# Kernel optimization log

Hardware: AMD Instinct MI355X
Metric: run time of the kernel (lower is better)

Reference implementation:

```python
import jax, jax.numpy as jnp
import numpy as np

T, B, F = 256, 128, 1600
H1, H2, H3 = 60, 15, 10   # MLP dims
GH = 5                    # GRU hidden size


def setup_inputs() -> dict:
    key = jax.random.key(0)
    ks = jax.random.split(key, 24)
    s = 0.1
    inp = {
        "X":   jax.random.normal(ks[0], (T, B, F), jnp.float32),
        "W1":  jax.random.normal(ks[1], (H1, F), jnp.float32) * s,
        "b1":  jax.random.normal(ks[2], (H1,), jnp.float32) * s,
        "W2":  jax.random.normal(ks[3], (H2, H1), jnp.float32) * s,
        "b2":  jax.random.normal(ks[4], (H2,), jnp.float32) * s,
        "W3":  jax.random.normal(ks[5], (H3, H2), jnp.float32) * s,
        "b3":  jax.random.normal(ks[6], (H3,), jnp.float32) * s,
    }
    in_sizes = [H3, GH, GH]
    k = 7
    for l in range(3):
        inp[f"w_ih{l}"] = jax.random.normal(ks[k], (3 * GH, in_sizes[l]), jnp.float32) * s; k += 1
        inp[f"w_hh{l}"] = jax.random.normal(ks[k], (3 * GH, GH), jnp.float32) * s; k += 1
        inp[f"b_ih{l}"] = jax.random.normal(ks[k], (3 * GH,), jnp.float32) * s; k += 1
        inp[f"b_hh{l}"] = jax.random.normal(ks[k], (3 * GH,), jnp.float32) * s; k += 1
    inp["Wout"] = jax.random.normal(ks[k], (1, GH), jnp.float32) * s; k += 1
    inp["bout"] = jax.random.normal(ks[k], (1,), jnp.float32) * s
    return inp


def _gru_layer(x, w_ih, w_hh, b_ih, b_hh):
    # x: (Bb, Tt, I). Precompute input-side gates for all timesteps.
    gi = jnp.einsum('bti,gi->btg', x, w_ih) + b_ih  # (Bb, Tt, 3H)

    def step(h_prev, gi_t):
        gh = h_prev @ w_hh.T + b_hh                 # (Bb, 3H)
        ir, iz, in_ = jnp.split(gi_t, 3, axis=-1)
        hr, hz, hn = jnp.split(gh, 3, axis=-1)
        r = jax.nn.sigmoid(ir + hr)
        z = jax.nn.sigmoid(iz + hz)
        n = jnp.tanh(in_ + r * hn)
        h = (1.0 - z) * n + z * h_prev
        return h, h

    h0 = jnp.zeros((x.shape[0], w_hh.shape[1]), x.dtype)
    _, ys = jax.lax.scan(step, h0, jnp.swapaxes(gi, 0, 1))  # (Tt, Bb, H)
    return jnp.swapaxes(ys, 0, 1)                            # (Bb, Tt, H)


def reference(X, W1, b1, W2, b2, W3, b3,
              w_ih0, w_hh0, b_ih0, b_hh0,
              w_ih1, w_hh1, b_ih1, b_hh1,
              w_ih2, w_hh2, b_ih2, b_hh2,
              Wout, bout):
    x = jnp.transpose(X, (1, 0, 2))        # (B, T, 1600): GRU batch_first layout
    h = jnp.tanh(x @ W1.T + b1)
    h = jnp.tanh(h @ W2.T + b2)
    h = h @ W3.T + b3                      # (B, T, 10) -- no activation after last MLP layer
    seq = h
    for p in ((w_ih0, w_hh0, b_ih0, b_hh0),
              (w_ih1, w_hh1, b_ih1, b_hh1),
              (w_ih2, w_hh2, b_ih2, b_hh2)):
        seq = _gru_layer(seq, *p)          # (B, T, 5)
    y = jnp.swapaxes(seq, 0, 1)            # (T, B, 5)
    y = y @ Wout.T + bout                  # (T, B, 1)
    return jnp.swapaxes(y, -1, -2)         # (T, 1, B)
```

## Files before the change

### kernel.cpp

```cpp
#include <hip/hip_runtime.h>
#include <hip/hip_bf16.h>


#define T_DIM 256
#define B_DIM 128
#define F_DIM 1600
#define H1_DIM 60
#define H2_DIM 15
#define H3_DIM 10
#define GH 5
#define NSTEP 50
#define CT 32
#define NCH (T_DIM / CT)

#define DPP_SHR5  0x115
#define DPP_SHR10 0x11A

typedef __attribute__((ext_vector_type(8))) short bf16x8;
typedef __attribute__((ext_vector_type(4))) float f32x4;

__device__ __forceinline__ float fast_tanh(float x) {
    float e = __expf(2.0f * x);
    return 1.0f - __fdividef(2.0f, e + 1.0f);
}
__device__ __forceinline__ float fast_sigmoid(float x) {
    return __fdividef(1.0f, 1.0f + __expf(-x));
}
__device__ __forceinline__ ushort f2bf_rn(float x) {
    uint u = __float_as_uint(x);
    u += 0x7fffu + ((u >> 16) & 1u);
    return (ushort)(u >> 16);
}
template <int CTRL>
__device__ __forceinline__ float dppf(float v) {
    return __int_as_float(
        __builtin_amdgcn_mov_dpp(__float_as_int(v), CTRL, 0xf, 0xf, true));
}
__device__ __forceinline__ float bperm(int addr, float v) {
    return __int_as_float(__builtin_amdgcn_ds_bpermute(addr, __float_as_int(v)));
}

__global__ __launch_bounds__(256) void pack_w1_kernel(
    const float* __restrict__ W1, ushort* __restrict__ Wp)
{
    const int s  = blockIdx.x;
    const int t  = threadIdx.x;
    const int nf = t >> 6;
    const int l  = t & 63;
    const int n  = nf * 16 + (l & 15);
    const int g  = l >> 4;

    ushort hi[8], lo[8];
#pragma unroll
    for (int j = 0; j < 8; ++j) {
        const int k = s * 32 + g * 8 + j;
        const float v = (n < H1_DIM) ? W1[n * F_DIM + k] : 0.0f;
        const ushort h = f2bf_rn(v);
        const float hf = __uint_as_float(((uint)h) << 16);
        const float r  = v - hf;
        hi[j] = h;
        lo[j] = (ushort)(__float_as_uint(r) >> 16);
    }
    ushort* dst = Wp + ((size_t)(s * 8 + nf * 2)) * 512 + l * 8;
#pragma unroll
    for (int j = 0; j < 8; ++j) dst[j] = hi[j];
#pragma unroll
    for (int j = 0; j < 8; ++j) dst[512 + j] = lo[j];
}

__global__ __launch_bounds__(256) void mlp_kernel(
    const float* __restrict__ X,
    const ushort* __restrict__ Wp,
    const float* __restrict__ b1,
    const float* __restrict__ W2, const float* __restrict__ b2,
    const float* __restrict__ W3, const float* __restrict__ b3,
    const float* __restrict__ wih0, const float* __restrict__ bih0,
    float* __restrict__ gi0)
{
    __shared__ float redp[64 * 65];

    const int tid  = threadIdx.x;
    const int l    = tid & 63;
    const int w    = __builtin_amdgcn_readfirstlane(tid >> 6);
    const int lm   = l & 15;
    const int g    = l >> 4;
    const int row0 = blockIdx.x * 64;

    f32x4 acc[4];
#pragma unroll
    for (int nf = 0; nf < 4; ++nf)
        acc[nf] = (f32x4){0.f, 0.f, 0.f, 0.f};

    const float* ap = X + (size_t)(row0 + w * 16 + lm) * F_DIM + g * 8;

    float4 x0 = *(const float4*)(ap);
    float4 x1 = *(const float4*)(ap + 4);

    for (int s = 0; s < NSTEP; ++s) {
        float4 n0 = make_float4(0.f, 0.f, 0.f, 0.f);
        float4 n1 = n0;
        if (s + 1 < NSTEP) {
            n0 = *(const float4*)(ap + (s + 1) * 32);
            n1 = *(const float4*)(ap + (s + 1) * 32 + 4);
        }
        bf16x8 bh[4], bl[4];
        const ushort* wp_s = Wp + (size_t)s * 4096 + l * 8;
#pragma unroll
        for (int nf = 0; nf < 4; ++nf) {
            bh[nf] = *(const bf16x8*)(wp_s + (nf * 2 + 0) * 512);
            bl[nf] = *(const bf16x8*)(wp_s + (nf * 2 + 1) * 512);
        }
        const float xs8[8] = {x0.x, x0.y, x0.z, x0.w, x1.x, x1.y, x1.z, x1.w};
        bf16x8 ah, al;
#pragma unroll
        for (int j = 0; j < 8; ++j) {
            const float v = xs8[j];
            const uint  u = __float_as_uint(v);
            const uint uh = (u + 0x7fffu + ((u >> 16) & 1u)) & 0xffff0000u;
            const float hf = __uint_as_float(uh);
            const float r  = v - hf;
            ah[j] = (short)(uh >> 16);
            al[j] = (short)(__float_as_uint(r) >> 16);
        }
#pragma unroll
        for (int nf = 0; nf < 4; ++nf) {
            f32x4 c = acc[nf];
            c = __builtin_amdgcn_mfma_f32_16x16x32_bf16(al, bh[nf], c, 0, 0, 0);
            c = __builtin_amdgcn_mfma_f32_16x16x32_bf16(ah, bl[nf], c, 0, 0, 0);
            c = __builtin_amdgcn_mfma_f32_16x16x32_bf16(ah, bh[nf], c, 0, 0, 0);
            acc[nf] = c;
        }
        x0 = n0; x1 = n1;
    }

#pragma unroll
    for (int nf = 0; nf < 4; ++nf)
#pragma unroll
        for (int q = 0; q < 4; ++q)
            redp[(w * 16 + g * 4 + q) * 65 + nf * 16 + lm] = acc[nf][q];
    __syncthreads();
    if (w != 0) return;

    float h1v[H1_DIM];
#pragma unroll
    for (int o = 0; o < H1_DIM; ++o)
        h1v[o] = fast_tanh(redp[l * 65 + o] + b1[o]);

    float h2v[H2_DIM];
#pragma unroll
    for (int j = 0; j < H2_DIM; ++j) {
        float sacc = b2[j];
#pragma unroll
        for (int o = 0; o < H1_DIM; ++o) sacc += W2[j * H1_DIM + o] * h1v[o];
        h2v[j] = fast_tanh(sacc);
    }

    float h3v[H3_DIM];
#pragma unroll
    for (int m = 0; m < H3_DIM; ++m) {
        float sacc = b3[m];
#pragma unroll
        for (int j = 0; j < H2_DIM; ++j) sacc += W3[m * H2_DIM + j] * h2v[j];
        h3v[m] = sacc;
    }

    float gv[15];
#pragma unroll
    for (int q = 0; q < 15; ++q) {
        float sacc = bih0[q];
#pragma unroll
        for (int m = 0; m < H3_DIM; ++m) sacc += wih0[q * H3_DIM + m] * h3v[m];
        gv[q] = sacc;
    }

    const int row = row0 + l;
    float4* dst = (float4*)(gi0 + (size_t)row * 16);
    dst[0] = make_float4(gv[0],  gv[1],  gv[2],  gv[3]);
    dst[1] = make_float4(gv[4],  gv[5],  gv[6],  gv[7]);
    dst[2] = make_float4(gv[8],  gv[9],  gv[10], gv[11]);
    dst[3] = make_float4(gv[12], gv[13], gv[14], 0.0f);
}


#define STAGE(C) do {                                                       \
    const int _cb = (C) & 1;                                                \
    float4 _v0, _v1;                                                        \
    {                                                                       \
        const int _t = lane >> 2, _q = lane & 3;                            \
        _v0 = *(const float4*)(gi0 +                                        \
            ((size_t)(((C) * CT + _t) * B_DIM + b)) * 16 + _q * 4);         \
    }                                                                       \
    {                                                                       \
        const int _f = lane + 64, _t = _f >> 2, _q = _f & 3;                \
        _v1 = *(const float4*)(gi0 +                                        \
            ((size_t)(((C) * CT + _t) * B_DIM + b)) * 16 + _q * 4);         \
    }                                                                       \
    *(float4*)&gbuf[_cb][lane >> 2][(lane & 3) * 4] = _v0;                  \
    *(float4*)&gbuf[_cb][(lane + 64) >> 2][((lane + 64) & 3) * 4] = _v1;    \
} while (0)

#define PREF(CB, TL) do { pre = lptr[(CB) * (CT * 16) + (TL) * 16]; } while (0)

#define GSTEP(S, PREFCODE) do {                                             \
         \
    float aA = bA + pre;                                                    \
    _Pragma("unroll") for (int _j = 0; _j < GH; ++_j)                       \
        aA = fmaf(wi[_j], xn[_j], aA);                                      \
    float aB = fmaf(wh[0], hn[0], bB);                                      \
    _Pragma("unroll") for (int _j = 1; _j < GH; ++_j)                       \
        aB = fmaf(wh[_j], hn[_j], aB);                                      \
    PREFCODE                                                                \
    const float sAv = aA + aB;                                              \
    const float sg  = fast_sigmoid(sAv);                                    \
    const float rn  = dppf<DPP_SHR10>(sg);        \
    const float zn  = dppf<DPP_SHR5>(sg);         \
    if (lane == 48 && (unsigned)((S) - 3) < (unsigned)T_DIM)                \
        out[((S) - 3) * B_DIM + b] = sAv;    \
    const float nv = fast_tanh(fmaf(rn, aB, aA));                           \
    const float hu = fmaf(zn, hm - nv, nv);                                 \
    const bool _valid = (unsigned)((S) - row) < (unsigned)T_DIM;            \
    hm = _valid ? hu : hm;                                                  \
                  \
    _Pragma("unroll") for (int _j = 0; _j < GH; ++_j) {                     \
        hn[_j] = bperm(a_self[_j], hm);                                     \
        xn[_j] = bperm(a_prev[_j], hm);                                     \
    }                                                                       \
} while (0)

__global__ __launch_bounds__(128, 1) void gru_kernel(
    const float* __restrict__ gi0,
    const float* __restrict__ whh0, const float* __restrict__ bhh0,
    const float* __restrict__ wih1, const float* __restrict__ whh1,
    const float* __restrict__ bih1, const float* __restrict__ bhh1,
    const float* __restrict__ wih2, const float* __restrict__ whh2,
    const float* __restrict__ bih2, const float* __restrict__ bhh2,
    const float* __restrict__ Wout, const float* __restrict__ bout,
    float* __restrict__ out)
{
    __shared__ float gbuf[2][CT][16];

    const int tid  = threadIdx.x;
    const int w    = __builtin_amdgcn_readfirstlane(tid >> 6);
    const int lane = tid & 63;
    const int b    = blockIdx.x;

    if (w == 1) {
        STAGE(0);
        __syncthreads();
        for (int c = 0; c < NCH; ++c) {
            if (c + 1 < NCH) STAGE(c + 1);
            __syncthreads();
        }
        return;
    }

    const int row = lane >> 4;
    const int g   = lane & 15;

    float wi[GH], wh[GH];
    float bA = 0.f, bB = 0.f;
#pragma unroll
    for (int j = 0; j < GH; ++j) { wi[j] = 0.f; wh[j] = 0.f; }

    if (row == 0) {
        if (g < 15) {
#pragma unroll
            for (int j = 0; j < GH; ++j) wh[j] = whh0[g * GH + j];
            bB = bhh0[g];
        }
    } else if (row < 3) {
        const float* wip = (row == 1) ? wih1 : wih2;
        const float* whp = (row == 1) ? whh1 : whh2;
        const float* bip = (row == 1) ? bih1 : bih2;
        const float* bhp = (row == 1) ? bhh1 : bhh2;
        if (g < 15) {
#pragma unroll
            for (int j = 0; j < GH; ++j) {
                wi[j] = wip[g * GH + j];
                wh[j] = whp[g * GH + j];
            }
            bA = bip[g];
            bB = bhp[g];
        }
    } else if (g == 0) {
#pragma unroll
        for (int j = 0; j < GH; ++j) wi[j] = Wout[j];
        bA = bout[0];
    }

    int a_self[GH], a_prev[GH];
    const int sbase = row * 16;
    const int pbase = ((row + 3) & 3) * 16;
#pragma unroll
    for (int j = 0; j < GH; ++j) {
        a_self[j] = (sbase + 10 + j) << 2;
        a_prev[j] = (pbase + 10 + j) << 2;
    }

    const float* lptr = &gbuf[0][0][(row == 0) ? g : 15];

    float hn[GH] = {0.f, 0.f, 0.f, 0.f, 0.f};
    float xn[GH] = {0.f, 0.f, 0.f, 0.f, 0.f};
    float hm = 0.f, pre = 0.f;

    __syncthreads();
    PREF(0, 0);

    for (int c = 0; c < NCH; ++c) {
        const int cb = c & 1;
#pragma unroll 2
        for (int tl = 0; tl < CT; ++tl) {
            const int s = c * CT + tl;
            GSTEP(s, if (tl + 1 < CT) { PREF(cb, tl + 1); });
        }
        __syncthreads();
        if (c + 1 < NCH) { PREF((c + 1) & 1, 0); }
    }

    for (int s = T_DIM; s < T_DIM + 3; ++s) {
        GSTEP(s, ;);
    }
}

extern "C" void kernel_launch(void* const* d_in, const int* in_sizes, int n_in,
                              void* d_out, int out_size, void* d_ws, size_t ws_size,
                              hipStream_t stream)
{
    (void)in_sizes; (void)n_in; (void)out_size; (void)ws_size;

    const float* X    = (const float*)d_in[0];
    const float* W1   = (const float*)d_in[1];
    const float* b1   = (const float*)d_in[2];
    const float* W2   = (const float*)d_in[3];
    const float* b2   = (const float*)d_in[4];
    const float* W3   = (const float*)d_in[5];
    const float* b3   = (const float*)d_in[6];
    const float* wih0 = (const float*)d_in[7];
    const float* whh0 = (const float*)d_in[8];
    const float* bih0 = (const float*)d_in[9];
    const float* bhh0 = (const float*)d_in[10];
    const float* wih1 = (const float*)d_in[11];
    const float* whh1 = (const float*)d_in[12];
    const float* bih1 = (const float*)d_in[13];
    const float* bhh1 = (const float*)d_in[14];
    const float* wih2 = (const float*)d_in[15];
    const float* whh2 = (const float*)d_in[16];
    const float* bih2 = (const float*)d_in[17];
    const float* bhh2 = (const float*)d_in[18];
    const float* Wout = (const float*)d_in[19];
    const float* bout = (const float*)d_in[20];

    ushort* Wp  = (ushort*)d_ws;
    float*  gi0 = (float*)((char*)d_ws + 524288);

    pack_w1_kernel<<<NSTEP, 256, 0, stream>>>(W1, Wp);
    mlp_kernel<<<512, 256, 0, stream>>>(X, Wp, b1, W2, b2, W3, b3, wih0, bih0, gi0);
    gru_kernel<<<128, 128, 0, stream>>>(gi0, whh0, bhh0,
                                        wih1, whh1, bih1, bhh1,
                                        wih2, whh2, bih2, bhh2,
                                        Wout, bout, (float*)d_out);
}
```

Baseline: 128.7 us.

## Fuse MLP and GRU into one per-batch kernel with wave-specialized pipelining

Replaces the separate MLP and GRU kernels with one kernel per batch element of 640 threads. Eight waves compute the layer-1 GEMM for 32-timestep chunks, split four ways over K. A ninth wave reduces the partial sums and runs the small MLP tail into shared memory, while wave 0 runs the GRU recurrence on the previous chunk. This removes the gi0 global round trip and the launch boundary, and overlaps the GEMM with the serial recurrence. The cost is that the GEMM now runs on only 128 blocks with a three-stage, barrier-synchronised pipeline, which reduces GEMM parallelism across the GPU.

```diff
diff --git a/kernel.cpp b/kernel.cpp
--- a/kernel.cpp
+++ b/kernel.cpp
@@ -12,6 +12,8 @@
 #define NSTEP 50
 #define CT 32
 #define NCH (T_DIM / CT)
+#define PBSTR 68
+#define NPW 8
 
 #define DPP_SHR5  0x115
 #define DPP_SHR10 0x11A
@@ -67,137 +69,6 @@
 #pragma unroll
     for (int j = 0; j < 8; ++j) dst[512 + j] = lo[j];
 }
-
-__global__ __launch_bounds__(256) void mlp_kernel(
-    const float* __restrict__ X,
-    const ushort* __restrict__ Wp,
-    const float* __restrict__ b1,
-    const float* __restrict__ W2, const float* __restrict__ b2,
-    const float* __restrict__ W3, const float* __restrict__ b3,
-    const float* __restrict__ wih0, const float* __restrict__ bih0,
-    float* __restrict__ gi0)
-{
-    __shared__ float redp[64 * 65];
-
-    const int tid  = threadIdx.x;
-    const int l    = tid & 63;
-    const int w    = __builtin_amdgcn_readfirstlane(tid >> 6);
-    const int lm   = l & 15;
-    const int g    = l >> 4;
-    const int row0 = blockIdx.x * 64;
-
-    f32x4 acc[4];
-#pragma unroll
-    for (int nf = 0; nf < 4; ++nf)
-        acc[nf] = (f32x4){0.f, 0.f, 0.f, 0.f};
-
-    const float* ap = X + (size_t)(row0 + w * 16 + lm) * F_DIM + g * 8;
-
-    float4 x0 = *(const float4*)(ap);
-    float4 x1 = *(const float4*)(ap + 4);
-
-    for (int s = 0; s < NSTEP; ++s) {
-        float4 n0 = make_float4(0.f, 0.f, 0.f, 0.f);
-        float4 n1 = n0;
-        if (s + 1 < NSTEP) {
-            n0 = *(const float4*)(ap + (s + 1) * 32);
-            n1 = *(const float4*)(ap + (s + 1) * 32 + 4);
-        }
-        bf16x8 bh[4], bl[4];
-        const ushort* wp_s = Wp + (size_t)s * 4096 + l * 8;
-#pragma unroll
-        for (int nf = 0; nf < 4; ++nf) {
-            bh[nf] = *(const bf16x8*)(wp_s + (nf * 2 + 0) * 512);
-            bl[nf] = *(const bf16x8*)(wp_s + (nf * 2 + 1) * 512);
-        }
-        const float xs8[8] = {x0.x, x0.y, x0.z, x0.w, x1.x, x1.y, x1.z, x1.w};
-        bf16x8 ah, al;
-#pragma unroll
-        for (int j = 0; j < 8; ++j) {
-            const float v = xs8[j];
-            const uint  u = __float_as_uint(v);
-            const uint uh = (u + 0x7fffu + ((u >> 16) & 1u)) & 0xffff0000u;
-            const float hf = __uint_as_float(uh);
-            const float r  = v - hf;
-            ah[j] = (short)(uh >> 16);
-            al[j] = (short)(__float_as_uint(r) >> 16);
-        }
-#pragma unroll
-        for (int nf = 0; nf < 4; ++nf) {
-            f32x4 c = acc[nf];
-            c = __builtin_amdgcn_mfma_f32_16x16x32_bf16(al, bh[nf], c, 0, 0, 0);
-            c = __builtin_amdgcn_mfma_f32_16x16x32_bf16(ah, bl[nf], c, 0, 0, 0);
-            c = __builtin_amdgcn_mfma_f32_16x16x32_bf16(ah, bh[nf], c, 0, 0, 0);
-            acc[nf] = c;
-        }
-        x0 = n0; x1 = n1;
-    }
-
-#pragma unroll
-    for (int nf = 0; nf < 4; ++nf)
-#pragma unroll
-        for (int q = 0; q < 4; ++q)
-            redp[(w * 16 + g * 4 + q) * 65 + nf * 16 + lm] = acc[nf][q];
-    __syncthreads();
-    if (w != 0) return;
-
-    float h1v[H1_DIM];
-#pragma unroll
-    for (int o = 0; o < H1_DIM; ++o)
-        h1v[o] = fast_tanh(redp[l * 65 + o] + b1[o]);
-
-    float h2v[H2_DIM];
-#pragma unroll
-    for (int j = 0; j < H2_DIM; ++j) {
-        float sacc = b2[j];
-#pragma unroll
-        for (int o = 0; o < H1_DIM; ++o) sacc += W2[j * H1_DIM + o] * h1v[o];
-        h2v[j] = fast_tanh(sacc);
-    }
-
-    float h3v[H3_DIM];
-#pragma unroll
-    for (int m = 0; m < H3_DIM; ++m) {
-        float sacc = b3[m];
-#pragma unroll
-        for (int j = 0; j < H2_DIM; ++j) sacc += W3[m * H2_DIM + j] * h2v[j];
-        h3v[m] = sacc;
-    }
-
-    float gv[15];
-#pragma unroll
-    for (int q = 0; q < 15; ++q) {
-        float sacc = bih0[q];
-#pragma unroll
-        for (int m = 0; m < H3_DIM; ++m) sacc += wih0[q * H3_DIM + m] * h3v[m];
-        gv[q] = sacc;
-    }
-
-    const int row = row0 + l;
-    float4* dst = (float4*)(gi0 + (size_t)row * 16);
-    dst[0] = make_float4(gv[0],  gv[1],  gv[2],  gv[3]);
-    dst[1] = make_float4(gv[4],  gv[5],  gv[6],  gv[7]);
-    dst[2] = make_float4(gv[8],  gv[9],  gv[10], gv[11]);
-    dst[3] = make_float4(gv[12], gv[13], gv[14], 0.0f);
-}
-
-
-#define STAGE(C) do {                                                       \
-    const int _cb = (C) & 1;                                                \
-    float4 _v0, _v1;                                                        \
-    {                                                                       \
-        const int _t = lane >> 2, _q = lane & 3;                            \
-        _v0 = *(const float4*)(gi0 +                                        \
-            ((size_t)(((C) * CT + _t) * B_DIM + b)) * 16 + _q * 4);         \
-    }                                                                       \
-    {                                                                       \
-        const int _f = lane + 64, _t = _f >> 2, _q = _f & 3;                \
-        _v1 = *(const float4*)(gi0 +                                        \
-            ((size_t)(((C) * CT + _t) * B_DIM + b)) * 16 + _q * 4);         \
-    }                                                                       \
-    *(float4*)&gbuf[_cb][lane >> 2][(lane & 3) * 4] = _v0;                  \
-    *(float4*)&gbuf[_cb][(lane + 64) >> 2][((lane + 64) & 3) * 4] = _v1;    \
-} while (0)
 
 #define PREF(CB, TL) do { pre = lptr[(CB) * (CT * 16) + (TL) * 16]; } while (0)
 
@@ -227,8 +98,13 @@
     }                                                                       \
 } while (0)
 
-__global__ __launch_bounds__(128, 1) void gru_kernel(
-    const float* __restrict__ gi0,
+__global__ __launch_bounds__(640, 1) void fused_kernel(
+    const float* __restrict__ X,
+    const ushort* __restrict__ Wp,
+    const float* __restrict__ b1,
+    const float* __restrict__ W2, const float* __restrict__ b2,
+    const float* __restrict__ W3, const float* __restrict__ b3,
+    const float* __restrict__ wih0, const float* __restrict__ bih0,
     const float* __restrict__ whh0, const float* __restrict__ bhh0,
     const float* __restrict__ wih1, const float* __restrict__ whh1,
     const float* __restrict__ bih1, const float* __restrict__ bhh1,
@@ -237,88 +113,214 @@
     const float* __restrict__ Wout, const float* __restrict__ bout,
     float* __restrict__ out)
 {
+    __shared__ float PB[2][4][2][16 * PBSTR];
     __shared__ float gbuf[2][CT][16];
 
     const int tid  = threadIdx.x;
-    const int w    = __builtin_amdgcn_readfirstlane(tid >> 6);
+    const int wv   = __builtin_amdgcn_readfirstlane(tid >> 6);
     const int lane = tid & 63;
     const int b    = blockIdx.x;
 
-    if (w == 1) {
-        STAGE(0);
-        __syncthreads();
-        for (int c = 0; c < NCH; ++c) {
-            if (c + 1 < NCH) STAGE(c + 1);
+    if (wv == 0) {
+        const int row = lane >> 4;
+        const int g   = lane & 15;
+
+        float wi[GH], wh[GH];
+        float bA = 0.f, bB = 0.f;
+#pragma unroll
+        for (int j = 0; j < GH; ++j) { wi[j] = 0.f; wh[j] = 0.f; }
+
+        if (row == 0) {
+            if (g < 15) {
+#pragma unroll
+                for (int j = 0; j < GH; ++j) wh[j] = whh0[g * GH + j];
+                bB = bhh0[g];
+            }
+        } else if (row < 3) {
+            const float* wip = (row == 1) ? wih1 : wih2;
+            const float* whp = (row == 1) ? whh1 : whh2;
+            const float* bip = (row == 1) ? bih1 : bih2;
+            const float* bhp = (row == 1) ? bhh1 : bhh2;
+            if (g < 15) {
+#pragma unroll
+                for (int j = 0; j < GH; ++j) {
+                    wi[j] = wip[g * GH + j];
+                    wh[j] = whp[g * GH + j];
+                }
+                bA = bip[g];
+                bB = bhp[g];
+            }
+        } else if (g == 0) {
+#pragma unroll
+            for (int j = 0; j < GH; ++j) wi[j] = Wout[j];
+            bA = bout[0];
+        }
+
+        int a_self[GH], a_prev[GH];
+        const int sbase = row * 16;
+        const int pbase = ((row + 3) & 3) * 16;
+#pragma unroll
+        for (int j = 0; j < GH; ++j) {
+            a_self[j] = (sbase + 10 + j) << 2;
+            a_prev[j] = (pbase + 10 + j) << 2;
+        }
+
+        const float* lptr = &gbuf[0][0][(row == 0) ? g : 15];
+
+        float hn[GH] = {0.f, 0.f, 0.f, 0.f, 0.f};
+        float xn[GH] = {0.f, 0.f, 0.f, 0.f, 0.f};
+        float hm = 0.f, pre = 0.f;
+
+        for (int i = 0; i < NCH + 2; ++i) {
+            if (i >= 2) {
+                const int cc = i - 2;
+                const int cb = cc & 1;
+                PREF(cb, 0);
+#pragma unroll 2
+                for (int tl = 0; tl < CT; ++tl) {
+                    const int s = cc * CT + tl;
+                    GSTEP(s, if (tl + 1 < CT) { PREF(cb, tl + 1); });
+                }
+            }
             __syncthreads();
+        }
+        for (int s = T_DIM; s < T_DIM + 3; ++s) {
+            GSTEP(s, ;);
         }
         return;
     }
 
-    const int row = lane >> 4;
-    const int g   = lane & 15;
-
-    float wi[GH], wh[GH];
-    float bA = 0.f, bB = 0.f;
-#pragma unroll
-    for (int j = 0; j < GH; ++j) { wi[j] = 0.f; wh[j] = 0.f; }
-
-    if (row == 0) {
-        if (g < 15) {
-#pragma unroll
-            for (int j = 0; j < GH; ++j) wh[j] = whh0[g * GH + j];
-            bB = bhh0[g];
-        }
-    } else if (row < 3) {
-        const float* wip = (row == 1) ? wih1 : wih2;
-        const float* whp = (row == 1) ? whh1 : whh2;
-        const float* bip = (row == 1) ? bih1 : bih2;
-        const float* bhp = (row == 1) ? bhh1 : bhh2;
-        if (g < 15) {
-#pragma unroll
-            for (int j = 0; j < GH; ++j) {
-                wi[j] = wip[g * GH + j];
-                wh[j] = whp[g * GH + j];
-            }
-            bA = bip[g];
-            bB = bhp[g];
-        }
-    } else if (g == 0) {
-#pragma unroll
-        for (int j = 0; j < GH; ++j) wi[j] = Wout[j];
-        bA = bout[0];
+    if (wv <= NPW) {
+        const int q  = (wv - 1) & 3;
+        const int mf = (wv - 1) >> 2;
+        const int lm = lane & 15;
+        const int g  = lane >> 4;
+        const int s0 = (q * NSTEP) >> 2;
+        const int s1 = ((q + 1) * NSTEP) >> 2;
+
+        for (int i = 0; i < NCH + 2; ++i) {
+            if (i < NCH) {
+                const float* ap = X
+                    + (size_t)((i * CT + mf * 16 + lm) * B_DIM + b) * F_DIM
+                    + s0 * 32 + g * 8;
+
+                f32x4 acc[4];
+#pragma unroll
+                for (int nf = 0; nf < 4; ++nf)
+                    acc[nf] = (f32x4){0.f, 0.f, 0.f, 0.f};
+
+                float4 x0 = *(const float4*)(ap);
+                float4 x1 = *(const float4*)(ap + 4);
+
+                for (int s = s0; s < s1; ++s) {
+                    float4 n0 = make_float4(0.f, 0.f, 0.f, 0.f);
+                    float4 n1 = n0;
+                    if (s + 1 < s1) {
+                        n0 = *(const float4*)(ap + (s + 1 - s0) * 32);
+                        n1 = *(const float4*)(ap + (s + 1 - s0) * 32 + 4);
+                    }
+                    bf16x8 bh[4], bl[4];
+                    const ushort* wp_s = Wp + (size_t)s * 4096 + lane * 8;
+#pragma unroll
+                    for (int nf = 0; nf < 4; ++nf) {
+                        bh[nf] = *(const bf16x8*)(wp_s + (nf * 2 + 0) * 512);
+                        bl[nf] = *(const bf16x8*)(wp_s + (nf * 2 + 1) * 512);
+                    }
+                    const float xs8[8] = {x0.x, x0.y, x0.z, x0.w,
+                                          x1.x, x1.y, x1.z, x1.w};
+                    bf16x8 ah, al;
+#pragma unroll
+                    for (int j = 0; j < 8; ++j) {
+                        const float v = xs8[j];
+                        const uint  u = __float_as_uint(v);
+                        const uint uh = (u + 0x7fffu + ((u >> 16) & 1u)) & 0xffff0000u;
+                        const float hf = __uint_as_float(uh);
+                        const float r  = v - hf;
+                        ah[j] = (short)(uh >> 16);
+                        al[j] = (short)(__float_as_uint(r) >> 16);
+                    }
+#pragma unroll
+                    for (int nf = 0; nf < 4; ++nf) {
+                        f32x4 c = acc[nf];
+                        c = __builtin_amdgcn_mfma_f32_16x16x32_bf16(al, bh[nf], c, 0, 0, 0);
+                        c = __builtin_amdgcn_mfma_f32_16x16x32_bf16(ah, bl[nf], c, 0, 0, 0);
+                        c = __builtin_amdgcn_mfma_f32_16x16x32_bf16(ah, bh[nf], c, 0, 0, 0);
+                        acc[nf] = c;
+                    }
+                    x0 = n0; x1 = n1;
+                }
+
+                float* myred = &PB[i & 1][q][mf][0];
+#pragma unroll
+                for (int nf = 0; nf < 4; ++nf)
+#pragma unroll
+                    for (int qq = 0; qq < 4; ++qq)
+                        myred[(g * 4 + qq) * PBSTR + nf * 16 + lm] = acc[nf][qq];
+            }
+            __syncthreads();
+        }
+        return;
     }
 
-    int a_self[GH], a_prev[GH];
-    const int sbase = row * 16;
-    const int pbase = ((row + 3) & 3) * 16;
-#pragma unroll
-    for (int j = 0; j < GH; ++j) {
-        a_self[j] = (sbase + 10 + j) << 2;
-        a_prev[j] = (pbase + 10 + j) << 2;
-    }
-
-    const float* lptr = &gbuf[0][0][(row == 0) ? g : 15];
-
-    float hn[GH] = {0.f, 0.f, 0.f, 0.f, 0.f};
-    float xn[GH] = {0.f, 0.f, 0.f, 0.f, 0.f};
-    float hm = 0.f, pre = 0.f;
-
-    __syncthreads();
-    PREF(0, 0);
-
-    for (int c = 0; c < NCH; ++c) {
-        const int cb = c & 1;
-#pragma unroll 2
-        for (int tl = 0; tl < CT; ++tl) {
-            const int s = c * CT + tl;
-            GSTEP(s, if (tl + 1 < CT) { PREF(cb, tl + 1); });
+    for (int i = 0; i < NCH + 2; ++i) {
+        if (i >= 1 && i <= NCH && lane < 32) {
+            const int cc = i - 1;
+            const int cb = cc & 1;
+            const int mf = lane >> 4, rr = lane & 15;
+
+            float s60[H1_DIM];
+            const float4* p0 = (const float4*)&PB[cb][0][mf][rr * PBSTR];
+            const float4* p1 = (const float4*)&PB[cb][1][mf][rr * PBSTR];
+            const float4* p2 = (const float4*)&PB[cb][2][mf][rr * PBSTR];
+            const float4* p3 = (const float4*)&PB[cb][3][mf][rr * PBSTR];
+#pragma unroll
+            for (int o4 = 0; o4 < 15; ++o4) {
+                const float4 a = p0[o4], bq = p1[o4], cq = p2[o4], dq = p3[o4];
+                s60[o4 * 4 + 0] = (a.x + bq.x) + (cq.x + dq.x);
+                s60[o4 * 4 + 1] = (a.y + bq.y) + (cq.y + dq.y);
+                s60[o4 * 4 + 2] = (a.z + bq.z) + (cq.z + dq.z);
+                s60[o4 * 4 + 3] = (a.w + bq.w) + (cq.w + dq.w);
+            }
+
+            float h1v[H1_DIM];
+#pragma unroll
+            for (int o = 0; o < H1_DIM; ++o)
+                h1v[o] = fast_tanh(s60[o] + b1[o]);
+
+            float h2v[H2_DIM];
+#pragma unroll
+            for (int j = 0; j < H2_DIM; ++j) {
+                float sacc = b2[j];
+#pragma unroll
+                for (int o = 0; o < H1_DIM; ++o) sacc += W2[j * H1_DIM + o] * h1v[o];
+                h2v[j] = fast_tanh(sacc);
+            }
+
+            float h3v[H3_DIM];
+#pragma unroll
+            for (int m = 0; m < H3_DIM; ++m) {
+                float sacc = b3[m];
+#pragma unroll
+                for (int j = 0; j < H2_DIM; ++j) sacc += W3[m * H2_DIM + j] * h2v[j];
+                h3v[m] = sacc;
+            }
+
+            float gv[15];
+#pragma unroll
+            for (int qy = 0; qy < 15; ++qy) {
+                float sacc = bih0[qy];
+#pragma unroll
+                for (int m = 0; m < H3_DIM; ++m) sacc += wih0[qy * H3_DIM + m] * h3v[m];
+                gv[qy] = sacc;
+            }
+
+            float4* dst = (float4*)&gbuf[cb][lane][0];
+            dst[0] = make_float4(gv[0],  gv[1],  gv[2],  gv[3]);
+            dst[1] = make_float4(gv[4],  gv[5],  gv[6],  gv[7]);
+            dst[2] = make_float4(gv[8],  gv[9],  gv[10], gv[11]);
+            dst[3] = make_float4(gv[12], gv[13], gv[14], 0.0f);
         }
         __syncthreads();
-        if (c + 1 < NCH) { PREF((c + 1) & 1, 0); }
-    }
-
-    for (int s = T_DIM; s < T_DIM + 3; ++s) {
-        GSTEP(s, ;);
     }
 }
 
@@ -350,13 +352,12 @@
     const float* Wout = (const float*)d_in[19];
     const float* bout = (const float*)d_in[20];
 
-    ushort* Wp  = (ushort*)d_ws;
-    float*  gi0 = (float*)((char*)d_ws + 524288);
+    ushort* Wp = (ushort*)d_ws;
 
     pack_w1_kernel<<<NSTEP, 256, 0, stream>>>(W1, Wp);
-    mlp_kernel<<<512, 256, 0, stream>>>(X, Wp, b1, W2, b2, W3, b3, wih0, bih0, gi0);
-    gru_kernel<<<128, 128, 0, stream>>>(gi0, whh0, bhh0,
-                                        wih1, whh1, bih1, bhh1,
-                                        wih2, whh2, bih2, bhh2,
-                                        Wout, bout, (float*)d_out);
-}
+    fused_kernel<<<B_DIM, 640, 0, stream>>>(X, Wp, b1, W2, b2, W3, b3,
+                                            wih0, bih0, whh0, bhh0,
+                                            wih1, whh1, bih1, bhh1,
+                                            wih2, whh2, bih2, bhh2,
+                                            Wout, bout, (float*)d_out);
+}
```

Result: slower. 135.5 us (+5.3%).

## Split MLP K-dimension across waves and shorten GRU gate FMA chains

Applied to the files above, without the earlier changes.

Each MLP block now handles 16 rows and its four waves split the 1600-wide reduction into K-slices, then combine partial sums through shared memory. The grid grows from 512 to 2048 blocks to raise parallelism and latency hiding while streaming X. Separately, the GRU gate dot-products are restructured from serial FMA chains into a shallower tree to cut the per-step dependency latency on the recurrent critical path. The cost is an extra shared-memory reduction with two more barriers, only 16 lanes doing the MLP epilogue, and slightly different floating-point summation order.

```diff
diff --git a/kernel.cpp b/kernel.cpp
--- a/kernel.cpp
+++ b/kernel.cpp
@@ -77,31 +77,33 @@
     const float* __restrict__ wih0, const float* __restrict__ bih0,
     float* __restrict__ gi0)
 {
-    __shared__ float redp[64 * 65];
+    __shared__ float red[4][1024];
 
     const int tid  = threadIdx.x;
     const int l    = tid & 63;
     const int w    = __builtin_amdgcn_readfirstlane(tid >> 6);
     const int lm   = l & 15;
     const int g    = l >> 4;
-    const int row0 = blockIdx.x * 64;
+    const int row0 = blockIdx.x * 16;
 
     f32x4 acc[4];
 #pragma unroll
     for (int nf = 0; nf < 4; ++nf)
         acc[nf] = (f32x4){0.f, 0.f, 0.f, 0.f};
 
-    const float* ap = X + (size_t)(row0 + w * 16 + lm) * F_DIM + g * 8;
-
-    float4 x0 = *(const float4*)(ap);
+    const int s0 = (w * NSTEP) >> 2;
+    const int s1 = ((w + 1) * NSTEP) >> 2;
+
+    const float* ap = X + (size_t)(row0 + lm) * F_DIM + s0 * 32 + g * 8;
+    float4 x0 = *(const float4*)ap;
     float4 x1 = *(const float4*)(ap + 4);
 
-    for (int s = 0; s < NSTEP; ++s) {
+    for (int s = s0; s < s1; ++s) {
         float4 n0 = make_float4(0.f, 0.f, 0.f, 0.f);
         float4 n1 = n0;
-        if (s + 1 < NSTEP) {
-            n0 = *(const float4*)(ap + (s + 1) * 32);
-            n1 = *(const float4*)(ap + (s + 1) * 32 + 4);
+        if (s + 1 < s1) {
+            n0 = *(const float4*)(ap + (s + 1 - s0) * 32);
+            n1 = *(const float4*)(ap + (s + 1 - s0) * 32 + 4);
         }
         bf16x8 bh[4], bl[4];
         const ushort* wp_s = Wp + (size_t)s * 4096 + l * 8;
@@ -133,13 +135,29 @@
         x0 = n0; x1 = n1;
     }
 
+    float* myred = &red[w][0];
 #pragma unroll
     for (int nf = 0; nf < 4; ++nf)
 #pragma unroll
         for (int q = 0; q < 4; ++q)
-            redp[(w * 16 + g * 4 + q) * 65 + nf * 16 + lm] = acc[nf][q];
+            myred[(g * 4 + q) * 64 + nf * 16 + lm] = acc[nf][q];
     __syncthreads();
-    if (w != 0) return;
+
+    float rsum[4];
+#pragma unroll
+    for (int i = 0; i < 4; ++i) {
+        const int p = tid + 256 * i;
+        rsum[i] = red[0][p] + red[1][p] + red[2][p] + red[3][p];
+    }
+    __syncthreads();
+    float* redp = &red[2][0];
+#pragma unroll
+    for (int i = 0; i < 4; ++i) {
+        const int p = tid + 256 * i;
+        redp[(p >> 6) * 65 + (p & 63)] = rsum[i];
+    }
+    __syncthreads();
+    if (w != 0 || l >= 16) return;
 
     float h1v[H1_DIM];
 #pragma unroll
@@ -202,13 +220,19 @@
 #define PREF(CB, TL) do { pre = lptr[(CB) * (CT * 16) + (TL) * 16]; } while (0)
 
 #define GSTEP(S, PREFCODE) do {                                             \
-         \
-    float aA = bA + pre;                                                    \
-    _Pragma("unroll") for (int _j = 0; _j < GH; ++_j)                       \
-        aA = fmaf(wi[_j], xn[_j], aA);                                      \
-    float aB = fmaf(wh[0], hn[0], bB);                                      \
-    _Pragma("unroll") for (int _j = 1; _j < GH; ++_j)                       \
-        aB = fmaf(wh[_j], hn[_j], aB);                                      \
+             \
+    const float _i0 = fmaf(wi[0], xn[0], bA + pre);                         \
+    const float _i1 = wi[1] * xn[1];                                        \
+    const float _i2 = fmaf(wi[2], xn[2], _i1);                              \
+    const float _i3 = wi[3] * xn[3];                                        \
+    const float _i4 = fmaf(wi[4], xn[4], _i3);                              \
+    const float aA  = (_i0 + _i2) + _i4;                                    \
+    const float _u0 = fmaf(wh[0], hn[0], bB);                               \
+    const float _u1 = wh[1] * hn[1];                                        \
+    const float _u2 = fmaf(wh[2], hn[2], _u1);                              \
+    const float _u3 = wh[3] * hn[3];                                        \
+    const float _u4 = fmaf(wh[4], hn[4], _u3);                              \
+    const float aB  = (_u0 + _u2) + _u4;                                    \
     PREFCODE                                                                \
     const float sAv = aA + aB;                                              \
     const float sg  = fast_sigmoid(sAv);                                    \
@@ -354,7 +378,7 @@
     float*  gi0 = (float*)((char*)d_ws + 524288);
 
     pack_w1_kernel<<<NSTEP, 256, 0, stream>>>(W1, Wp);
-    mlp_kernel<<<512, 256, 0, stream>>>(X, Wp, b1, W2, b2, W3, b3, wih0, bih0, gi0);
+    mlp_kernel<<<2048, 256, 0, stream>>>(X, Wp, b1, W2, b2, W3, b3, wih0, bih0, gi0);
     gru_kernel<<<128, 128, 0, stream>>>(gi0, whh0, bhh0,
                                         wih1, whh1, bih1, bhh1,
                                         wih2, whh2, bih2, bhh2,
```

New measurement: 122.5 us. 4.9% less time.
